# Optimization experiments

Measured on AMD Instinct MI355X. Metric: run time of the kernel, lower is better.

The kernel has to match this reference:

```python
import jax, jax.numpy as jnp
import numpy as np
from itertools import product as iter_product

# ---- configuration (mirrors init_kwargs) ----
N_QUBITS = 14
BATCH = 128
INPUT_DIM = 256
PROJ_HIDDEN = 256            # max(256, enc_per_block // 2)
DEPTH = 4                    # vqc_depth
N_GEN = 15                   # (2**2)**2 - 1 generators per SU(4) gate
N_GROUPS = 13                # 7 even + 6 odd brick-layer groups for n=14, k=2
ENC_PER_BLOCK = N_GROUPS * N_GEN   # 195
N_OBS = N_QUBITS - 1         # sliding 2-local windows -> 13
CDTYPE = jnp.complex64


def _pauli_generators():
    I = np.eye(2)
    X = np.array([[0., 1.], [1., 0.]])
    Y = np.array([[0., -1j], [1j, 0.]])
    Z = np.array([[1., 0.], [0., -1.]])
    P = [I, X, Y, Z]
    gens = [np.kron(P[a], P[b]) for a, b in iter_product(range(4), repeat=2)
            if not (a == 0 and b == 0)]
    return jnp.asarray(np.stack(gens).astype(np.complex64))   # (15, 4, 4)

GENS2 = _pauli_generators()
SUN_STARTS = list(range(0, N_QUBITS - 1, 2)) + list(range(1, N_QUBITS - 2, 2))
OBS_STARTS = list(range(N_QUBITS - 1))
CNOT = jnp.asarray(np.array([[1, 0, 0, 0], [0, 1, 0, 0],
                             [0, 0, 0, 1], [0, 0, 1, 0]], np.complex64))
# lower-triangular fill order of create_Hermitian for N=4
_ROWS = np.array([1, 2, 2, 3, 3, 3])
_COLS = np.array([0, 0, 1, 0, 1, 2])


def _apply2_batched(state, U, q):
    """Apply per-batch 4x4 unitary U (B,4,4) on adjacent qubits (q, q+1)."""
    B = state.shape[0]
    s = state.reshape(B, 2 ** q, 4, -1)
    return jnp.einsum('bkl,bplq->bpkq', U, s).reshape(B, -1)


def _apply2_shared(state, U, q):
    B = state.shape[0]
    s = state.reshape(B, 2 ** q, 4, -1)
    return jnp.einsum('kl,bplq->bpkq', U, s).reshape(B, -1)


def _apply1_shared(state, U, q):
    B = state.shape[0]
    s = state.reshape(B, 2 ** q, 2, -1)
    return jnp.einsum('kl,bplq->bpkq', U, s).reshape(B, -1)


def _expval2(state, H, q):
    """<psi| H_{q,q+1} |psi> for 4x4 Hermitian H."""
    B = state.shape[0]
    s = state.reshape(B, 2 ** q, 4, -1)
    return jnp.einsum('bpkq,kl,bplq->b', jnp.conj(s), H, s).real


def _build_hermitians(obs_A, obs_B, obs_D):
    """create_Hermitian(4, A, B, D) for all observables, vectorized."""
    n_obs = obs_A.shape[0]
    h = jnp.zeros((n_obs, 4, 4), dtype=CDTYPE)
    h = h.at[:, _ROWS, _COLS].set((obs_A + 1j * obs_B).astype(CDTYPE))
    h = h.at[:, np.arange(3), np.arange(3)].set(obs_D[:, 1:4].astype(CDTYPE))
    return h + jnp.conj(jnp.swapaxes(h, -1, -2))


def setup_inputs() -> dict:
    key = jax.random.key(0)
    ks = jax.random.split(key, 8)
    x = jax.random.normal(ks[0], (BATCH, INPUT_DIM), jnp.float32)
    W1 = jax.random.normal(ks[1], (PROJ_HIDDEN, INPUT_DIM), jnp.float32) / np.sqrt(INPUT_DIM)
    b1 = jnp.zeros((PROJ_HIDDEN,), jnp.float32)
    W2 = jax.random.normal(ks[2], (ENC_PER_BLOCK, PROJ_HIDDEN), jnp.float32) / np.sqrt(PROJ_HIDDEN)
    b2 = jnp.zeros((ENC_PER_BLOCK,), jnp.float32)
    var_params = 0.01 * jax.random.normal(ks[3], (DEPTH, N_QUBITS), jnp.float32)
    obs_A = 2.0 * jax.random.normal(ks[4], (N_OBS, 6), jnp.float32)
    obs_B = 2.0 * jax.random.normal(ks[5], (N_OBS, 6), jnp.float32)
    obs_D = 2.0 * jax.random.normal(ks[6], (N_OBS, 4), jnp.float32)
    return {'x': x, 'W1': W1, 'b1': b1, 'W2': W2, 'b2': b2,
            'var_params': var_params, 'obs_A': obs_A, 'obs_B': obs_B, 'obs_D': obs_D}


def reference(x, W1, b1, W2, b2, var_params, obs_A, obs_B, obs_D):
    # classical encoder: Linear -> SiLU -> Linear
    enc = jax.nn.silu(x @ W1.T + b1) @ W2.T + b2          # (B, 195)
    B = x.shape[0]
    state = jnp.zeros((B, 2 ** N_QUBITS), dtype=CDTYPE).at[:, 0].set(1.0)

    # SU(4) brick-layer data encoding: U = exp(i * sum_g theta_g G_g)
    # A is Hermitian (real theta, Hermitian Paulis) -> exp via eigh.
    for g, q in enumerate(SUN_STARTS):
        theta = enc[:, g * N_GEN:(g + 1) * N_GEN].astype(CDTYPE)    # (B, 15)
        A = jnp.einsum('bg,gij->bij', theta, GENS2)                 # (B, 4, 4)
        w, V = jnp.linalg.eigh(A)
        phase = jnp.exp(1j * w.astype(CDTYPE))
        U = jnp.einsum('bik,bk,bjk->bij', V, phase, jnp.conj(V))
        state = _apply2_batched(state, U, q)

    # hardware-efficient variational ansatz: RY layer + CNOT chain, repeated
    half = 0.5 * var_params
    c, s = jnp.cos(half), jnp.sin(half)
    for d in range(DEPTH):
        for q in range(N_QUBITS):
            ry = jnp.stack([jnp.stack([c[d, q], -s[d, q]]),
                            jnp.stack([s[d, q], c[d, q]])]).astype(CDTYPE)
            state = _apply1_shared(state, ry, q)
        for q in range(N_QUBITS - 1):
            state = _apply2_shared(state, CNOT, q)

    # learnable 2-local Hermitian observables on sliding windows
    H = _build_hermitians(obs_A, obs_B, obs_D)            # (13, 4, 4)
    outs = [_expval2(state, H[i], q) for i, q in enumerate(OBS_STARTS)]
    return jnp.stack(outs, axis=1)                        # (B, 13)
```

## Files before the change

kernel.cpp:

```cpp
#include <hip/hip_runtime.h>
#include <math.h>

#define NQ        14
#define DIM       16384
#define BATCHN    128
#define NGATES    13
#define NGEN      15
#define NOBSN     13
#define DEPTHN    4
#define INDIM     256
#define HIDDIM    256
#define ENCDIM    195
#define TCIRC     1024

__constant__ float c_PR[4][2][2] = {
  {{1.f, 0.f}, {0.f, 1.f}},
  {{0.f, 1.f}, {1.f, 0.f}},
  {{0.f, 0.f}, {0.f, 0.f}},
  {{1.f, 0.f}, {0.f,-1.f}},
};
__constant__ float c_PI[4][2][2] = {
  {{0.f, 0.f}, {0.f, 0.f}},
  {{0.f, 0.f}, {0.f, 0.f}},
  {{0.f,-1.f}, {1.f, 0.f}},
  {{0.f, 0.f}, {0.f, 0.f}},
};

__device__ __forceinline__ float rfl(float x) {
  return __int_as_float(__builtin_amdgcn_readfirstlane(__float_as_int(x)));
}

constexpr int ef_c(int y) {
  return y ^ (((y >> 5) & 1) * 5)
           ^ (((y >> 6) & 1) * 18)
           ^ (((y >> 7) & 1) * 12)
           ^ (((y >> 8) & 1) * 8)
           ^ (((y >> 9) & 1) * 2);
}
constexpr int siginv_c(int z) {
  int t = z;
  t ^= t >> 1; t ^= t >> 2; t ^= t >> 4; t ^= t >> 8;
  return t & 16383;
}
constexpr int ymap_c(int i) {
  const int p3 = (i >> 3) & 1;
  const int p2 = p3 ^ ((i >> 2) & 1);
  const int p1 = p2 ^ ((i >> 1) & 1);
  const int p0 = p1 ^ (i & 1);
  return (p3 << 3) | (p2 << 2) | (p1 << 1) | p0;
}
constexpr int qidx(int MODE, int i, int s) {
  return MODE == 0 ? ((i << 2) | s)
       : MODE == 1 ? (((s >> 1) << 3) | (i << 1) | (s & 1))
       : ((s << 2) | i);
}

template<int MODE>
__device__ __forceinline__ float qform16(const float2* __restrict__ hp,
                                         const float vr[16], const float vi[16]) {
  const int ui[6] = {0, 0, 0, 1, 1, 2};
  const int uj[6] = {1, 2, 3, 2, 3, 3};
  float dH[4], oR[6], oI[6];
  #pragma unroll
  for (int i = 0; i < 4; ++i) dH[i] = rfl(hp[i * 5].x);
  #pragma unroll
  for (int u = 0; u < 6; ++u) {
    oR[u] = rfl(2.f * hp[ui[u] * 4 + uj[u]].x);
    oI[u] = rfl(2.f * hp[ui[u] * 4 + uj[u]].y);
  }
  float acc = 0.f;
  #pragma unroll
  for (int s = 0; s < 4; ++s) {
    #pragma unroll
    for (int i = 0; i < 4; ++i) {
      const int k = qidx(MODE, i, s);
      acc = fmaf(dH[i], fmaf(vr[k], vr[k], vi[k] * vi[k]), acc);
    }
    #pragma unroll
    for (int u = 0; u < 6; ++u) {
      const int a = qidx(MODE, ui[u], s), b2 = qidx(MODE, uj[u], s);
      const float p = fmaf(vr[a], vr[b2], vi[a] * vi[b2]);
      const float q = fmaf(vr[a], vi[b2], -(vi[a] * vr[b2]));
      acc = fmaf(oR[u], p, fmaf(-oI[u], q, acc));
    }
  }
  return acc;
}

__device__ __forceinline__ void init_productW(float2* __restrict__ st,
                                              const float2* __restrict__ Ush,
                                              int tid) {
  const int w = tid >> 6, l = tid & 63;
  const int k0 = w >> 2, k1 = w & 3;
  const int k2 = l >> 4, k3 = (l >> 2) & 3, k4 = l & 3;
  const float f0r = rfl(Ush[0 * 16 + k0 * 4].x), f0i = rfl(Ush[0 * 16 + k0 * 4].y);
  const float f1r = rfl(Ush[1 * 16 + k1 * 4].x), f1i = rfl(Ush[1 * 16 + k1 * 4].y);
  const float2 f2 = Ush[2 * 16 + k2 * 4];
  const float2 f3 = Ush[3 * 16 + k3 * 4];
  const float2 f4 = Ush[4 * 16 + k4 * 4];
  float hr = f0r * f1r - f0i * f1i, hi = f0r * f1i + f0i * f1r, tr, ti;
  tr = hr * f2.x - hi * f2.y; ti = hr * f2.y + hi * f2.x; hr = tr; hi = ti;
  tr = hr * f3.x - hi * f3.y; ti = hr * f3.y + hi * f3.x; hr = tr; hi = ti;
  tr = hr * f4.x - hi * f4.y; ti = hr * f4.y + hi * f4.x; hr = tr; hi = ti;
  float c5r[4], c5i[4], c6r[4], c6i[4];
  #pragma unroll
  for (int m = 0; m < 4; ++m) {
    c5r[m] = rfl(Ush[5 * 16 + m * 4].x); c5i[m] = rfl(Ush[5 * 16 + m * 4].y);
    c6r[m] = rfl(Ush[6 * 16 + m * 4].x); c6i[m] = rfl(Ush[6 * 16 + m * 4].y);
  }
  const int a0 = ef_c((w << 10) | (l << 4));
  #pragma unroll
  for (int k = 0; k < 16; ++k) {
    const float pr = c5r[k >> 2] * c6r[k & 3] - c5i[k >> 2] * c6i[k & 3];
    const float pi_ = c5r[k >> 2] * c6i[k & 3] + c5i[k >> 2] * c6r[k & 3];
    st[a0 ^ ef_c(k)] = make_float2(hr * pr - hi * pi_, hr * pi_ + hi * pr);
  }
}

__device__ __forceinline__ void gate_pair16(const float2* __restrict__ ugA,
                                            const float2* __restrict__ ugB,
                                            float vr[16], float vi[16]) {
  {
    float ur[16], ui_[16];
    #pragma unroll
    for (int i = 0; i < 16; ++i) { ur[i] = rfl(ugA[i].x); ui_[i] = rfl(ugA[i].y); }
    #pragma unroll
    for (int r = 0; r < 4; ++r) {
      float tr[4], ti_[4];
      #pragma unroll
      for (int i = 0; i < 4; ++i) {
        float sr = 0.f, si = 0.f;
        #pragma unroll
        for (int l = 0; l < 4; ++l) {
          const int kl = (l << 2) | r;
          sr = fmaf(ur[i * 4 + l], vr[kl], fmaf(-ui_[i * 4 + l], vi[kl], sr));
          si = fmaf(ur[i * 4 + l], vi[kl], fmaf(ui_[i * 4 + l], vr[kl], si));
        }
        tr[i] = sr; ti_[i] = si;
      }
      #pragma unroll
      for (int i = 0; i < 4; ++i) { vr[(i << 2) | r] = tr[i]; vi[(i << 2) | r] = ti_[i]; }
    }
  }
  {
    float ur[16], ui_[16];
    #pragma unroll
    for (int i = 0; i < 16; ++i) { ur[i] = rfl(ugB[i].x); ui_[i] = rfl(ugB[i].y); }
    #pragma unroll
    for (int r = 0; r < 4; ++r) {
      float tr[4], ti_[4];
      #pragma unroll
      for (int i = 0; i < 4; ++i) {
        float sr = 0.f, si = 0.f;
        #pragma unroll
        for (int l = 0; l < 4; ++l) {
          const int kl = (r << 2) | l;
          sr = fmaf(ur[i * 4 + l], vr[kl], fmaf(-ui_[i * 4 + l], vi[kl], sr));
          si = fmaf(ur[i * 4 + l], vi[kl], fmaf(ui_[i * 4 + l], vr[kl], si));
        }
        tr[i] = sr; ti_[i] = si;
      }
      #pragma unroll
      for (int i = 0; i < 4; ++i) { vr[(r << 2) | i] = tr[i]; vi[(r << 2) | i] = ti_[i]; }
    }
  }
}

template<int SH>
__device__ __forceinline__ void su4_pair(float2* __restrict__ st,
                                         const float2* __restrict__ ugA,
                                         const float2* __restrict__ ugB,
                                         int tid) {
  constexpr int m = (1 << SH) - 1;
  const int a0 = ef_c(((tid & ~m) << 4) | (tid & m));
  float vr[16], vi[16];
  #pragma unroll
  for (int k = 0; k < 16; ++k) {
    const float2 v = st[a0 ^ ef_c(k << SH)];
    vr[k] = v.x; vi[k] = v.y;
  }
  gate_pair16(ugA, ugB, vr, vi);
  #pragma unroll
  for (int k = 0; k < 16; ++k)
    st[a0 ^ ef_c(k << SH)] = make_float2(vr[k], vi[k]);
  __syncthreads();
}

template<int SH>
__device__ __forceinline__ void su4_pairW(float2* __restrict__ st,
                                          const float2* __restrict__ ugA,
                                          const float2* __restrict__ ugB,
                                          int tid) {
  const int w = tid >> 6, l = tid & 63;
  constexpr int m = (1 << SH) - 1;
  const int a0 = ef_c((w << 10) | ((l & ~m) << 4) | (l & m));
  float vr[16], vi[16];
  #pragma unroll
  for (int k = 0; k < 16; ++k) {
    const float2 v = st[a0 ^ ef_c(k << SH)];
    vr[k] = v.x; vi[k] = v.y;
  }
  gate_pair16(ugA, ugB, vr, vi);
  #pragma unroll
  for (int k = 0; k < 16; ++k)
    st[a0 ^ ef_c(k << SH)] = make_float2(vr[k], vi[k]);
}

template<int J>
__device__ __forceinline__ void bfly16(float c, float s, float pr[16], float pi_[16]) {
  #pragma unroll
  for (int i = 0; i < 16; ++i) {
    if ((i & (1 << J)) == 0) {
      const int j = i | (1 << J);
      const float ar = pr[i], ai = pi_[i], br = pr[j], bi = pi_[j];
      pr[i]  = fmaf(c, ar, -(s * br));
      pi_[i] = fmaf(c, ai, -(s * bi));
      pr[j]  = fmaf(s, ar, c * br);
      pi_[j] = fmaf(s, ai, c * bi);
    }
  }
}

template<int SH>
__device__ __forceinline__ void ry4W(float2* __restrict__ st,
                                     const float* __restrict__ rc,
                                     const float* __restrict__ rs, int tid) {
  const float c3 = rfl(rc[10 - SH]), s3 = rfl(rs[10 - SH]);
  const float c2 = rfl(rc[11 - SH]), s2 = rfl(rs[11 - SH]);
  const float c1 = rfl(rc[12 - SH]), s1 = rfl(rs[12 - SH]);
  const float c0 = rfl(rc[13 - SH]), s0 = rfl(rs[13 - SH]);
  const int w = tid >> 6, l = tid & 63;
  constexpr int m = (1 << SH) - 1;
  const int a0 = ef_c((w << 10) | ((l & ~m) << 4) | (l & m));
  float vr[16], vi[16];
  #pragma unroll
  for (int k = 0; k < 16; ++k) {
    const float2 v = st[a0 ^ ef_c(k << SH)];
    vr[k] = v.x; vi[k] = v.y;
  }
  bfly16<3>(c3, s3, vr, vi);
  bfly16<2>(c2, s2, vr, vi);
  bfly16<1>(c1, s1, vr, vi);
  bfly16<0>(c0, s0, vr, vi);
  #pragma unroll
  for (int k = 0; k < 16; ++k)
    st[a0 ^ ef_c(k << SH)] = make_float2(vr[k], vi[k]);
}

__device__ __forceinline__ void ry2W(float2* __restrict__ st,
                                     const float* __restrict__ rc,
                                     const float* __restrict__ rs, int tid) {
  const float c1 = rfl(rc[12]), s1 = rfl(rs[12]);
  const float c0 = rfl(rc[13]), s0 = rfl(rs[13]);
  const int w = tid >> 6, l = tid & 63;
  #pragma unroll
  for (int j = 0; j < 4; ++j) {
    const int a0 = ef_c((w << 10) | ((l + (j << 6)) << 2));
    float vr[4], vi[4];
    #pragma unroll
    for (int k = 0; k < 4; ++k) {
      const float2 v = st[a0 ^ ef_c(k)];
      vr[k] = v.x; vi[k] = v.y;
    }
    #pragma unroll
    for (int k = 0; k < 2; ++k) {
      const float ar = vr[k], ai = vi[k], br = vr[k + 2], bi = vi[k + 2];
      vr[k]     = fmaf(c1, ar, -(s1 * br));
      vi[k]     = fmaf(c1, ai, -(s1 * bi));
      vr[k + 2] = fmaf(s1, ar, c1 * br);
      vi[k + 2] = fmaf(s1, ai, c1 * bi);
    }
    #pragma unroll
    for (int k = 0; k < 4; k += 2) {
      const float ar = vr[k], ai = vi[k], br = vr[k + 1], bi = vi[k + 1];
      vr[k]     = fmaf(c0, ar, -(s0 * br));
      vi[k]     = fmaf(c0, ai, -(s0 * bi));
      vr[k + 1] = fmaf(s0, ar, c0 * br);
      vi[k + 1] = fmaf(s0, ai, c0 * bi);
    }
    #pragma unroll
    for (int k = 0; k < 4; ++k)
      st[a0 ^ ef_c(k)] = make_float2(vr[k], vi[k]);
  }
}

__device__ __forceinline__ void reduce_store(float a, float* slot, int lane, int wid) {
  #pragma unroll
  for (int off = 32; off > 0; off >>= 1)
    a += __shfl_down(a, off, 64);
  if (lane == 0) slot[wid] = a;
}

template<bool FINAL>
__device__ __forceinline__ void perm_ry_pass(float2* __restrict__ st,
                                             const float* __restrict__ rc,
                                             const float* __restrict__ rs,
                                             int tid,
                                             const float2* __restrict__ Hsh,
                                             float (*red)[TCIRC / 64],
                                             int lane, int wid) {
  const float c0 = rfl(rc[0]), s0 = rfl(rs[0]);
  const float c1 = rfl(rc[1]), s1 = rfl(rs[1]);
  const float c2 = rfl(rc[2]), s2 = rfl(rs[2]);
  const float c3 = rfl(rc[3]), s3 = rfl(rs[3]);
  __syncthreads();
  const int Er = ef_c(tid);
  float pr[16], pi_[16];
  #pragma unroll
  for (int i = 0; i < 16; ++i) {
    const float2 v = st[Er ^ ef_c(i << 10)];
    pr[i] = v.x; pi_[i] = v.y;
  }
  __syncthreads();
  bfly16<3>(c0, s0, pr, pi_);
  bfly16<2>(c1, s1, pr, pi_);
  bfly16<1>(c2, s2, pr, pi_);
  bfly16<0>(c3, s3, pr, pi_);
  if (FINAL) {
    float wr[16], wi[16];
    #pragma unroll
    for (int i = 0; i < 16; ++i) { wr[ymap_c(i)] = pr[i]; wi[ymap_c(i)] = pi_[i]; }
    reduce_store(qform16<0>(Hsh + 0 * 16, wr, wi), red[0], lane, wid);
    reduce_store(qform16<1>(Hsh + 1 * 16, wr, wi), red[1], lane, wid);
  }
  const int Ew = ef_c(siginv_c(tid));
  #pragma unroll
  for (int i = 0; i < 16; ++i)
    st[Ew ^ ef_c(siginv_c(i << 10))] = make_float2(pr[i], pi_[i]);
  __syncthreads();
}

template<int SH, int NOB>
__device__ __forceinline__ void obs_tri(const float2* __restrict__ st,
                                        const float2* __restrict__ Hsh, int obase,
                                        float (*red)[TCIRC / 64],
                                        int lane, int wid, int tid) {
  constexpr int m = (1 << SH) - 1;
  const int a0 = ef_c(((tid & ~m) << 4) | (tid & m));
  float vr[16], vi[16];
  #pragma unroll
  for (int k = 0; k < 16; ++k) {
    const float2 v = st[a0 ^ ef_c(k << SH)];
    vr[k] = v.x; vi[k] = v.y;
  }
  if (NOB == 3) {
    reduce_store(qform16<0>(Hsh + (obase + 0) * 16, vr, vi), red[obase + 0], lane, wid);
    reduce_store(qform16<1>(Hsh + (obase + 1) * 16, vr, vi), red[obase + 1], lane, wid);
    reduce_store(qform16<2>(Hsh + (obase + 2) * 16, vr, vi), red[obase + 2], lane, wid);
  } else {
    reduce_store(qform16<1>(Hsh + (obase + 0) * 16, vr, vi), red[obase + 0], lane, wid);
    reduce_store(qform16<2>(Hsh + (obase + 1) * 16, vr, vi), red[obase + 1], lane, wid);
  }
}

__launch_bounds__(TCIRC, 1)
__global__ void circuit_kernel(const float* __restrict__ x,
                               const float* __restrict__ W1,
                               const float* __restrict__ b1,
                               const float* __restrict__ W2,
                               const float* __restrict__ b2,
                               const float* __restrict__ vp,
                               const float* __restrict__ oA,
                               const float* __restrict__ oB,
                               const float* __restrict__ oD,
                               float* __restrict__ out) {
  __shared__ float2 st[DIM];
  __shared__ float2 Ush[NGATES * 16];
  __shared__ float2 Hsh[NOBSN * 16];
  __shared__ float  ryc[DEPTHN * NQ];
  __shared__ float  rys[DEPTHN * NQ];
  __shared__ float  red[NOBSN][TCIRC / 64];

  const int b = blockIdx.x;
  const int tid = threadIdx.x;

  float* base = (float*)st;
  float* xrow = base;
  float* hrow = base + 256;
  float* encs = base + 512;
  float* part = base + 1024;

  if (tid >= 960 && tid < 960 + DEPTHN * NQ) {
    const int i = tid - 960;
    const float h = 0.5f * vp[i];
    ryc[i] = cosf(h); rys[i] = sinf(h);
  }
  if (tid >= 832 && tid < 832 + NOBSN) {
    const int o = tid - 832;
    const int rr[6] = {1, 2, 2, 3, 3, 3};
    const int cc[6] = {0, 0, 1, 0, 1, 2};
    float2 H[16];
    #pragma unroll
    for (int i = 0; i < 16; ++i) H[i] = make_float2(0.f, 0.f);
    for (int m = 0; m < 6; ++m) {
      const float a = oA[o * 6 + m], bb = oB[o * 6 + m];
      H[rr[m] * 4 + cc[m]] = make_float2(a, bb);
      H[cc[m] * 4 + rr[m]] = make_float2(a, -bb);
    }
    H[0]  = make_float2(2.f * oD[o * 4 + 1], 0.f);
    H[5]  = make_float2(2.f * oD[o * 4 + 2], 0.f);
    H[10] = make_float2(2.f * oD[o * 4 + 3], 0.f);
    for (int i = 0; i < 16; ++i) Hsh[o * 16 + i] = H[i];
  }
  if (tid < INDIM) xrow[tid] = x[b * INDIM + tid];
  __syncthreads();

  {
    const int o = tid & 255, q = tid >> 8;
    const float4* wp = (const float4*)(W1 + o * INDIM + q * 64);
    const float4* xq = (const float4*)(xrow + q * 64);
    float a = 0.f;
    #pragma unroll 4
    for (int k = 0; k < 16; ++k) {
      const float4 wv = wp[k], xv = xq[k];
      a = fmaf(wv.x, xv.x, fmaf(wv.y, xv.y, fmaf(wv.z, xv.z, fmaf(wv.w, xv.w, a))));
    }
    part[(q << 8) | o] = a;
  }
  __syncthreads();
  if (tid < HIDDIM) {
    const float a = b1[tid] + part[tid] + part[256 + tid] + part[512 + tid] + part[768 + tid];
    hrow[tid] = a / (1.f + expf(-a));
  }
  __syncthreads();
  {
    const int o = tid & 255, q = tid >> 8;
    if (o < ENCDIM) {
      const float4* wp = (const float4*)(W2 + o * HIDDIM + q * 64);
      const float4* hq = (const float4*)(hrow + q * 64);
      float a = 0.f;
      #pragma unroll 4
      for (int k = 0; k < 16; ++k) {
        const float4 wv = wp[k], hv = hq[k];
        a = fmaf(wv.x, hv.x, fmaf(wv.y, hv.y, fmaf(wv.z, hv.z, fmaf(wv.w, hv.w, a))));
      }
      part[(q << 8) | o] = a;
    }
  }
  __syncthreads();
  if (tid < ENCDIM)
    encs[tid] = b2[tid] + part[tid] + part[256 + tid] + part[512 + tid] + part[768 + tid];
  __syncthreads();

  if (tid < NGATES * 16) {
    const int g = tid >> 4, e = tid & 15, i = e >> 2, j = e & 3;
    const float* th = encs + g * NGEN;
    float Are = 0.f, Aie = 0.f;
    for (int t = 0; t < NGEN; ++t) {
      const int p = t + 1;
      const int pa = p >> 2, pb = p & 3;
      const float ar = c_PR[pa][i >> 1][j >> 1], ai = c_PI[pa][i >> 1][j >> 1];
      const float br = c_PR[pb][i & 1][j & 1],  bi = c_PI[pb][i & 1][j & 1];
      Are = fmaf(th[t], ar * br - ai * bi, Are);
      Aie = fmaf(th[t], ar * bi + ai * br, Aie);
    }
    float r = sqrtf(Are * Are + Aie * Aie);
    r += __shfl_xor(r, 1, 16);
    r += __shfl_xor(r, 2, 16);
    float nrm = r;
    nrm = fmaxf(nrm, __shfl_xor(nrm, 4, 16));
    nrm = fmaxf(nrm, __shfl_xor(nrm, 8, 16));
    int sct = 0;
    float scale = 1.f;
    while (nrm * scale > 0.5f && sct < 30) { scale *= 0.5f; ++sct; }
    const float Mre = -Aie * scale, Mie = Are * scale;
    float Rr = (i == j) ? 1.f : 0.f, Ri = 0.f;
    for (int k = 10; k >= 1; --k) {
      const float inv = 1.f / (float)k;
      float tr = 0.f, ti = 0.f;
      #pragma unroll
      for (int l = 0; l < 4; ++l) {
        const float mr = __shfl(Mre, i * 4 + l, 16), mi = __shfl(Mie, i * 4 + l, 16);
        const float rr2 = __shfl(Rr, l * 4 + j, 16), ri2 = __shfl(Ri, l * 4 + j, 16);
        tr = fmaf(mr, rr2, fmaf(-mi, ri2, tr));
        ti = fmaf(mr, ri2, fmaf(mi, rr2, ti));
      }
      Rr = ((i == j) ? 1.f : 0.f) + inv * tr;
      Ri = inv * ti;
    }
    for (int it = 0; it < sct; ++it) {
      float tr = 0.f, ti = 0.f;
      #pragma unroll
      for (int l = 0; l < 4; ++l) {
        const float ar = __shfl(Rr, i * 4 + l, 16), ai2 = __shfl(Ri, i * 4 + l, 16);
        const float br = __shfl(Rr, l * 4 + j, 16), bi2 = __shfl(Ri, l * 4 + j, 16);
        tr = fmaf(ar, br, fmaf(-ai2, bi2, tr));
        ti = fmaf(ar, bi2, fmaf(ai2, br, ti));
      }
      Rr = tr; Ri = ti;
    }
    Ush[g * 16 + e] = make_float2(Rr, Ri);
  }
  __syncthreads();

  init_productW(st, Ush, tid);
  __syncthreads();

  su4_pair<9>(st, Ush + 7 * 16, Ush + 8 * 16, tid);
  su4_pairW<5>(st, Ush + 9 * 16, Ush + 10 * 16, tid);
  su4_pairW<1>(st, Ush + 11 * 16, Ush + 12 * 16, tid);

  const int lane = tid & 63, wid = tid >> 6;
  #pragma unroll 1
  for (int d = 0; d < DEPTHN - 1; ++d) {
    const float* rc = ryc + d * NQ;
    const float* rs = rys + d * NQ;
    ry4W<6>(st, rc, rs, tid);
    ry4W<2>(st, rc, rs, tid);
    ry2W(st, rc, rs, tid);
    perm_ry_pass<false>(st, rc, rs, tid, Hsh, red, lane, wid);
  }
  {
    const float* rc = ryc + (DEPTHN - 1) * NQ;
    const float* rs = rys + (DEPTHN - 1) * NQ;
    ry4W<6>(st, rc, rs, tid);
    ry4W<2>(st, rc, rs, tid);
    ry2W(st, rc, rs, tid);
    perm_ry_pass<true>(st, rc, rs, tid, Hsh, red, lane, wid);
  }

  obs_tri<8, 3>(st, Hsh, 2, red, lane, wid, tid);
  obs_tri<5, 3>(st, Hsh, 5, red, lane, wid, tid);
  obs_tri<2, 3>(st, Hsh, 8, red, lane, wid, tid);
  obs_tri<0, 2>(st, Hsh, 11, red, lane, wid, tid);

  __syncthreads();
  if (tid < NOBSN) {
    float s = 0.f;
    #pragma unroll
    for (int w = 0; w < TCIRC / 64; ++w) s += red[tid][w];
    out[b * NOBSN + tid] = s;
  }
}

extern "C" void kernel_launch(void* const* d_in, const int* in_sizes, int n_in,
                              void* d_out, int out_size, void* d_ws, size_t ws_size,
                              hipStream_t stream) {
  const float* x  = (const float*)d_in[0];
  const float* W1 = (const float*)d_in[1];
  const float* b1 = (const float*)d_in[2];
  const float* W2 = (const float*)d_in[3];
  const float* b2 = (const float*)d_in[4];
  const float* vp = (const float*)d_in[5];
  const float* oA = (const float*)d_in[6];
  const float* oB = (const float*)d_in[7];
  const float* oD = (const float*)d_in[8];
  float* out = (float*)d_out;

  circuit_kernel<<<BATCHN, TCIRC, 0, stream>>>(x, W1, b1, W2, b2, vp, oA, oB, oD, out);
}
```

Measured before the change: 80.43 us.

## Fuse product-state init into first SU4 pass and merge RY passes via DPP

The product-state initialisation is now computed directly in registers in the layout the first SU(4) gate pair needs. The gate is applied before writing, which removes one LDS write/read round trip and one barrier. The separate 2-qubit RY pass is folded into the second 4-qubit RY pass: the two lowest qubits live across adjacent lanes and are rotated with DPP lane swaps (quad_perm 0xB1 and 0x4E), removing another full shared-memory sweep. The cost is extra cross-lane DPP moves and more register pressure in the fused routines.

```diff
diff --git a/kernel.cpp b/kernel.cpp
--- a/kernel.cpp
+++ b/kernel.cpp
@@ -30,6 +30,11 @@
   return __int_as_float(__builtin_amdgcn_readfirstlane(__float_as_int(x)));
 }
 
+template<int CTRL>
+__device__ __forceinline__ float fdpp(float v) {
+  return __int_as_float(__builtin_amdgcn_mov_dpp(__float_as_int(v), CTRL, 0xF, 0xF, true));
+}
+
 constexpr int ef_c(int y) {
   return y ^ (((y >> 5) & 1) * 5)
            ^ (((y >> 6) & 1) * 18)
@@ -85,36 +90,6 @@
     }
   }
   return acc;
-}
-
-__device__ __forceinline__ void init_productW(float2* __restrict__ st,
-                                              const float2* __restrict__ Ush,
-                                              int tid) {
-  const int w = tid >> 6, l = tid & 63;
-  const int k0 = w >> 2, k1 = w & 3;
-  const int k2 = l >> 4, k3 = (l >> 2) & 3, k4 = l & 3;
-  const float f0r = rfl(Ush[0 * 16 + k0 * 4].x), f0i = rfl(Ush[0 * 16 + k0 * 4].y);
-  const float f1r = rfl(Ush[1 * 16 + k1 * 4].x), f1i = rfl(Ush[1 * 16 + k1 * 4].y);
-  const float2 f2 = Ush[2 * 16 + k2 * 4];
-  const float2 f3 = Ush[3 * 16 + k3 * 4];
-  const float2 f4 = Ush[4 * 16 + k4 * 4];
-  float hr = f0r * f1r - f0i * f1i, hi = f0r * f1i + f0i * f1r, tr, ti;
-  tr = hr * f2.x - hi * f2.y; ti = hr * f2.y + hi * f2.x; hr = tr; hi = ti;
-  tr = hr * f3.x - hi * f3.y; ti = hr * f3.y + hi * f3.x; hr = tr; hi = ti;
-  tr = hr * f4.x - hi * f4.y; ti = hr * f4.y + hi * f4.x; hr = tr; hi = ti;
-  float c5r[4], c5i[4], c6r[4], c6i[4];
-  #pragma unroll
-  for (int m = 0; m < 4; ++m) {
-    c5r[m] = rfl(Ush[5 * 16 + m * 4].x); c5i[m] = rfl(Ush[5 * 16 + m * 4].y);
-    c6r[m] = rfl(Ush[6 * 16 + m * 4].x); c6i[m] = rfl(Ush[6 * 16 + m * 4].y);
-  }
-  const int a0 = ef_c((w << 10) | (l << 4));
-  #pragma unroll
-  for (int k = 0; k < 16; ++k) {
-    const float pr = c5r[k >> 2] * c6r[k & 3] - c5i[k >> 2] * c6i[k & 3];
-    const float pi_ = c5r[k >> 2] * c6i[k & 3] + c5i[k >> 2] * c6r[k & 3];
-    st[a0 ^ ef_c(k)] = make_float2(hr * pr - hi * pi_, hr * pi_ + hi * pr);
-  }
 }
 
 __device__ __forceinline__ void gate_pair16(const float2* __restrict__ ugA,
@@ -166,23 +141,58 @@
   }
 }
 
-template<int SH>
-__device__ __forceinline__ void su4_pair(float2* __restrict__ st,
-                                         const float2* __restrict__ ugA,
-                                         const float2* __restrict__ ugB,
-                                         int tid) {
-  constexpr int m = (1 << SH) - 1;
+__device__ __forceinline__ void init_pair9(float2* __restrict__ st,
+                                           const float2* __restrict__ Ush,
+                                           int tid) {
+  const int t9 = (tid >> 9) & 1, t8 = (tid >> 8) & 1;
+  const int t76 = (tid >> 6) & 3;
+  const int t54 = (tid >> 4) & 3, t32 = (tid >> 2) & 3, t10 = tid & 3;
+  float f0r[2], f0i[2];
+  #pragma unroll
+  for (int k3 = 0; k3 < 2; ++k3) {
+    f0r[k3] = rfl(Ush[0 * 16 + ((t9 << 1) | k3) * 4].x);
+    f0i[k3] = rfl(Ush[0 * 16 + ((t9 << 1) | k3) * 4].y);
+  }
+  float f1r[4], f1i[4];
+  #pragma unroll
+  for (int j = 0; j < 4; ++j) {
+    f1r[j] = rfl(Ush[1 * 16 + j * 4].x);
+    f1i[j] = rfl(Ush[1 * 16 + j * 4].y);
+  }
+  float f2r[2], f2i[2];
+  #pragma unroll
+  for (int k0 = 0; k0 < 2; ++k0) {
+    f2r[k0] = rfl(Ush[2 * 16 + ((k0 << 1) | t8) * 4].x);
+    f2i[k0] = rfl(Ush[2 * 16 + ((k0 << 1) | t8) * 4].y);
+  }
+  const float f3r = rfl(Ush[3 * 16 + t76 * 4].x), f3i = rfl(Ush[3 * 16 + t76 * 4].y);
+  const float2 f4 = Ush[4 * 16 + t54 * 4];
+  const float2 f5 = Ush[5 * 16 + t32 * 4];
+  const float2 f6 = Ush[6 * 16 + t10 * 4];
+  float cr = f3r * f4.x - f3i * f4.y, ci = f3r * f4.y + f3i * f4.x, tr, ti;
+  tr = cr * f5.x - ci * f5.y; ti = cr * f5.y + ci * f5.x; cr = tr; ci = ti;
+  tr = cr * f6.x - ci * f6.y; ti = cr * f6.y + ci * f6.x; cr = tr; ci = ti;
+  float g2r[2], g2i[2];
+  #pragma unroll
+  for (int k0 = 0; k0 < 2; ++k0) {
+    g2r[k0] = f2r[k0] * cr - f2i[k0] * ci;
+    g2i[k0] = f2r[k0] * ci + f2i[k0] * cr;
+  }
+  float vr[16], vi[16];
+  #pragma unroll
+  for (int k = 0; k < 16; ++k) {
+    const int k3 = k >> 3, k21 = (k >> 1) & 3, k0 = k & 1;
+    const float hr2 = f0r[k3] * f1r[k21] - f0i[k3] * f1i[k21];
+    const float hi2 = f0r[k3] * f1i[k21] + f0i[k3] * f1r[k21];
+    vr[k] = hr2 * g2r[k0] - hi2 * g2i[k0];
+    vi[k] = hr2 * g2i[k0] + hi2 * g2r[k0];
+  }
+  gate_pair16(Ush + 7 * 16, Ush + 8 * 16, vr, vi);
+  constexpr int m = (1 << 9) - 1;
   const int a0 = ef_c(((tid & ~m) << 4) | (tid & m));
-  float vr[16], vi[16];
-  #pragma unroll
-  for (int k = 0; k < 16; ++k) {
-    const float2 v = st[a0 ^ ef_c(k << SH)];
-    vr[k] = v.x; vi[k] = v.y;
-  }
-  gate_pair16(ugA, ugB, vr, vi);
   #pragma unroll
   for (int k = 0; k < 16; ++k)
-    st[a0 ^ ef_c(k << SH)] = make_float2(vr[k], vi[k]);
+    st[a0 ^ ef_c(k << 9)] = make_float2(vr[k], vi[k]);
   __syncthreads();
 }
 
@@ -221,21 +231,19 @@
   }
 }
 
-template<int SH>
-__device__ __forceinline__ void ry4W(float2* __restrict__ st,
-                                     const float* __restrict__ rc,
-                                     const float* __restrict__ rs, int tid) {
-  const float c3 = rfl(rc[10 - SH]), s3 = rfl(rs[10 - SH]);
-  const float c2 = rfl(rc[11 - SH]), s2 = rfl(rs[11 - SH]);
-  const float c1 = rfl(rc[12 - SH]), s1 = rfl(rs[12 - SH]);
-  const float c0 = rfl(rc[13 - SH]), s0 = rfl(rs[13 - SH]);
+__device__ __forceinline__ void ry4W6(float2* __restrict__ st,
+                                      const float* __restrict__ rc,
+                                      const float* __restrict__ rs, int tid) {
+  const float c3 = rfl(rc[4]), s3 = rfl(rs[4]);
+  const float c2 = rfl(rc[5]), s2 = rfl(rs[5]);
+  const float c1 = rfl(rc[6]), s1 = rfl(rs[6]);
+  const float c0 = rfl(rc[7]), s0 = rfl(rs[7]);
   const int w = tid >> 6, l = tid & 63;
-  constexpr int m = (1 << SH) - 1;
-  const int a0 = ef_c((w << 10) | ((l & ~m) << 4) | (l & m));
+  const int a0 = ef_c((w << 10) | l);
   float vr[16], vi[16];
   #pragma unroll
   for (int k = 0; k < 16; ++k) {
-    const float2 v = st[a0 ^ ef_c(k << SH)];
+    const float2 v = st[a0 ^ ef_c(k << 6)];
     vr[k] = v.x; vi[k] = v.y;
   }
   bfly16<3>(c3, s3, vr, vi);
@@ -244,44 +252,51 @@
   bfly16<0>(c0, s0, vr, vi);
   #pragma unroll
   for (int k = 0; k < 16; ++k)
-    st[a0 ^ ef_c(k << SH)] = make_float2(vr[k], vi[k]);
-}
-
-__device__ __forceinline__ void ry2W(float2* __restrict__ st,
-                                     const float* __restrict__ rc,
-                                     const float* __restrict__ rs, int tid) {
-  const float c1 = rfl(rc[12]), s1 = rfl(rs[12]);
-  const float c0 = rfl(rc[13]), s0 = rfl(rs[13]);
+    st[a0 ^ ef_c(k << 6)] = make_float2(vr[k], vi[k]);
+}
+
+__device__ __forceinline__ void ry4W2d(float2* __restrict__ st,
+                                       const float* __restrict__ rc,
+                                       const float* __restrict__ rs, int tid) {
+  const float c3 = rfl(rc[8]),  s3 = rfl(rs[8]);
+  const float c2 = rfl(rc[9]),  s2 = rfl(rs[9]);
+  const float c1 = rfl(rc[10]), s1 = rfl(rs[10]);
+  const float c0 = rfl(rc[11]), s0 = rfl(rs[11]);
+  const float cA = rfl(rc[12]), sA = rfl(rs[12]);
+  const float cB = rfl(rc[13]), sB = rfl(rs[13]);
   const int w = tid >> 6, l = tid & 63;
-  #pragma unroll
-  for (int j = 0; j < 4; ++j) {
-    const int a0 = ef_c((w << 10) | ((l + (j << 6)) << 2));
-    float vr[4], vi[4];
-    #pragma unroll
-    for (int k = 0; k < 4; ++k) {
-      const float2 v = st[a0 ^ ef_c(k)];
-      vr[k] = v.x; vi[k] = v.y;
-    }
-    #pragma unroll
-    for (int k = 0; k < 2; ++k) {
-      const float ar = vr[k], ai = vi[k], br = vr[k + 2], bi = vi[k + 2];
-      vr[k]     = fmaf(c1, ar, -(s1 * br));
-      vi[k]     = fmaf(c1, ai, -(s1 * bi));
-      vr[k + 2] = fmaf(s1, ar, c1 * br);
-      vi[k + 2] = fmaf(s1, ai, c1 * bi);
-    }
-    #pragma unroll
-    for (int k = 0; k < 4; k += 2) {
-      const float ar = vr[k], ai = vi[k], br = vr[k + 1], bi = vi[k + 1];
-      vr[k]     = fmaf(c0, ar, -(s0 * br));
-      vi[k]     = fmaf(c0, ai, -(s0 * bi));
-      vr[k + 1] = fmaf(s0, ar, c0 * br);
-      vi[k + 1] = fmaf(s0, ai, c0 * bi);
-    }
-    #pragma unroll
-    for (int k = 0; k < 4; ++k)
-      st[a0 ^ ef_c(k)] = make_float2(vr[k], vi[k]);
-  }
+  const int a0 = ef_c((w << 10) | ((l & ~3) << 4) | (l & 3));
+  float vr[16], vi[16];
+  #pragma unroll
+  for (int k = 0; k < 16; ++k) {
+    const float2 v = st[a0 ^ ef_c(k << 2)];
+    vr[k] = v.x; vi[k] = v.y;
+  }
+  bfly16<3>(c3, s3, vr, vi);
+  bfly16<2>(c2, s2, vr, vi);
+  bfly16<1>(c1, s1, vr, vi);
+  bfly16<0>(c0, s0, vr, vi);
+  {
+    const float se = (l & 1) ? sB : -sB;
+    #pragma unroll
+    for (int k = 0; k < 16; ++k) {
+      const float pr = fdpp<0xB1>(vr[k]), pi_ = fdpp<0xB1>(vi[k]);
+      vr[k] = fmaf(cB, vr[k], se * pr);
+      vi[k] = fmaf(cB, vi[k], se * pi_);
+    }
+  }
+  {
+    const float se = (l & 2) ? sA : -sA;
+    #pragma unroll
+    for (int k = 0; k < 16; ++k) {
+      const float pr = fdpp<0x4E>(vr[k]), pi_ = fdpp<0x4E>(vi[k]);
+      vr[k] = fmaf(cA, vr[k], se * pr);
+      vi[k] = fmaf(cA, vi[k], se * pi_);
+    }
+  }
+  #pragma unroll
+  for (int k = 0; k < 16; ++k)
+    st[a0 ^ ef_c(k << 2)] = make_float2(vr[k], vi[k]);
 }
 
 __device__ __forceinline__ void reduce_store(float a, float* slot, int lane, int wid) {
@@ -493,10 +508,8 @@
   }
   __syncthreads();
 
-  init_productW(st, Ush, tid);
-  __syncthreads();
-
-  su4_pair<9>(st, Ush + 7 * 16, Ush + 8 * 16, tid);
+  init_pair9(st, Ush, tid);
+
   su4_pairW<5>(st, Ush + 9 * 16, Ush + 10 * 16, tid);
   su4_pairW<1>(st, Ush + 11 * 16, Ush + 12 * 16, tid);
 
@@ -505,17 +518,15 @@
   for (int d = 0; d < DEPTHN - 1; ++d) {
     const float* rc = ryc + d * NQ;
     const float* rs = rys + d * NQ;
-    ry4W<6>(st, rc, rs, tid);
-    ry4W<2>(st, rc, rs, tid);
-    ry2W(st, rc, rs, tid);
+    ry4W6(st, rc, rs, tid);
+    ry4W2d(st, rc, rs, tid);
     perm_ry_pass<false>(st, rc, rs, tid, Hsh, red, lane, wid);
   }
   {
     const float* rc = ryc + (DEPTHN - 1) * NQ;
     const float* rs = rys + (DEPTHN - 1) * NQ;
-    ry4W<6>(st, rc, rs, tid);
-    ry4W<2>(st, rc, rs, tid);
-    ry2W(st, rc, rs, tid);
+    ry4W6(st, rc, rs, tid);
+    ry4W2d(st, rc, rs, tid);
     perm_ry_pass<true>(st, rc, rs, tid, Hsh, red, lane, wid);
   }
 
```

After: 74.02 us. 8.0% less time.
